# Optimization experiments

Hardware: AMD Instinct MI355X
Metric: run time of the kernel (lower is better)

## Reference

```python
import jax, jax.numpy as jnp
import numpy as np
import math

NUM_HEADS = 12
BLOCK_N = 32  # key-block size used by the Triton kernel for head_dim <= 64


def _apply_rope(x, cos, sin):
    # x: [B,H,S,D]; cos/sin: [S, D//2] -> interleaved-pair RoPE (matches apply_rope_rse)
    c = cos[None, None, :, :]
    s = sin[None, None, :, :]
    xe = x[..., 0::2]
    xo = x[..., 1::2]
    re = xe * c - xo * s
    ro = xo * c + xe * s
    return jnp.stack([re, ro], axis=-1).reshape(x.shape)


def setup_inputs() -> dict:
    key = jax.random.key(0)
    ks = jax.random.split(key, 9)
    B, S, HID = 16, 1024, 768
    D = HID // NUM_HEADS
    x = jax.random.normal(ks[0], (B, S, HID), jnp.float32)
    init = lambda k: jax.random.normal(k, (HID, HID), jnp.float32) * 0.02
    Wq, Wk, Wv, Wo = init(ks[1]), init(ks[2]), init(ks[3]), init(ks[4])
    bq = jnp.zeros((HID,), jnp.float32)
    bk = jnp.zeros((HID,), jnp.float32)
    bv = jnp.zeros((HID,), jnp.float32)
    bo = jnp.zeros((HID,), jnp.float32)
    lam = jnp.array(0.01, jnp.float32)
    # RoPE caches [S, D//2]
    inv_freq = 1.0 / (10000.0 ** (jnp.arange(0, D, 2, dtype=jnp.float32) / D))
    ang = jnp.arange(S, dtype=jnp.float32)[:, None] * inv_freq[None, :]
    cos_cache = jnp.cos(ang)
    sin_cache = jnp.sin(ang)
    return {"x": x, "Wq": Wq, "bq": bq, "Wk": Wk, "bk": bk, "Wv": Wv, "bv": bv,
            "Wo": Wo, "bo": bo, "lam": lam, "cos_cache": cos_cache, "sin_cache": sin_cache}


def _rse_attention(q, k, v, cos_cache, sin_cache, lam):
    # q,k,v: [B,H,S,D]. Block-sequential stick-breaking with online stats,
    # faithfully reproducing the Triton kernel's math (causal=False).
    B, H, S, D = q.shape
    scale = 1.0 / math.sqrt(D)
    qs = _apply_rope(q, cos_cache, sin_cache) * scale
    kr = _apply_rope(k, cos_cache, sin_cache)
    nb = S // BLOCK_N
    kb = jnp.moveaxis(kr.reshape(B, H, nb, BLOCK_N, D), 2, 0)  # [nb,B,H,BN,D]
    vb = jnp.moveaxis(v.reshape(B, H, nb, BLOCK_N, D), 2, 0)   # [nb,B,H,BN,D]
    pos_m = jnp.arange(S, dtype=jnp.float32)
    pb = jnp.arange(S, dtype=jnp.float32).reshape(nb, BLOCK_N)

    def step(carry, inp):
        rem, acc, l_i, m_i = carry
        kblk, vblk, pblk = inp
        decay = lam * jnp.abs(pos_m[:, None] - pblk[None, :])  # [S,BN]
        logits = jnp.einsum('bhmd,bhnd->bhmn', qs, kblk) - decay[None, None]
        beta = jax.nn.sigmoid(jnp.clip(logits, -20.0, 20.0))
        w = beta * rem[..., None]                 # [B,H,S,BN]
        consumed = jnp.sum(w, axis=-1)            # [B,H,S]
        rem_new = jnp.maximum(rem * (1.0 - consumed), 1e-6)
        acc_new = acc + jnp.einsum('bhmn,bhnd->bhmd', w, vblk)
        m_new = jnp.maximum(m_i, jnp.max(logits, axis=-1))
        alpha = jnp.exp2(m_i - m_new)
        l_new = l_i * alpha + consumed
        return (rem_new, acc_new, l_new, m_new), None

    rem0 = jnp.ones((B, H, S), jnp.float32)
    acc0 = jnp.zeros((B, H, S, D), jnp.float32)
    l0 = jnp.zeros((B, H, S), jnp.float32)
    m0 = jnp.full((B, H, S), -jnp.inf, jnp.float32)
    (rem, acc, l_i, m_i), _ = jax.lax.scan(step, (rem0, acc0, l0, m0), (kb, vb, pb))
    return acc / jnp.maximum(l_i, 1e-6)[..., None]


def reference(x, Wq, bq, Wk, bk, Wv, bv, Wo, bo, lam, cos_cache, sin_cache):
    B, S, HID = x.shape
    H = NUM_HEADS
    D = HID // H
    to_heads = lambda t: t.reshape(B, S, H, D).transpose(0, 2, 1, 3)
    q = to_heads(x @ Wq.T + bq)
    k = to_heads(x @ Wk.T + bk)
    v = to_heads(x @ Wv.T + bv)
    o = _rse_attention(q, k, v, cos_cache, sin_cache, lam)  # [B,H,S,D]
    ctx = o.transpose(0, 2, 1, 3).reshape(B, S, HID)
    return ctx @ Wo.T + bo
```

## Files before the change

### kernel.cpp

```cpp
#include <hip/hip_runtime.h>
#include <math.h>

#define NH    12
#define SEQ   1024
#define DH    64
#define HID   768
#define BATCH 16
#define MTOT  (BATCH*SEQ)
#define KDIM  HID

typedef __attribute__((ext_vector_type(8))) short short8;
typedef __attribute__((ext_vector_type(4))) short short4v;
typedef __attribute__((ext_vector_type(8))) unsigned short ushort8;
typedef __attribute__((ext_vector_type(4))) float float4v;

__device__ __forceinline__ float bf2f(unsigned short u) {
    union { unsigned int i; float f; } v; v.i = ((unsigned int)u) << 16; return v.f;
}
__device__ __forceinline__ unsigned short f2bf(float f) {
    union { float f; unsigned int i; } v; v.f = f;
    unsigned int x = v.i;
    return (unsigned short)((x + 0x7FFFu + ((x >> 16) & 1u)) >> 16);
}
__device__ __forceinline__ float loadf(const void* p, size_t i, bool f32) {
    return f32 ? ((const float*)p)[i] : bf2f(((const unsigned short*)p)[i]);
}
__device__ __forceinline__ unsigned int cvt_pk_bf16(float a, float b) {
    unsigned int r;
    asm("v_cvt_pk_bf16_f32 %0, %1, %2" : "=v"(r) : "v"(a), "v"(b));
    return r;
}
__device__ __forceinline__ float fast_exp2(float x) {
#if __has_builtin(__builtin_amdgcn_exp2f)
    return __builtin_amdgcn_exp2f(x);
#else
    return exp2f(x);
#endif
}

__device__ __forceinline__ void gload_lds16(const void* g, void* l) {
    __builtin_amdgcn_global_load_lds(
        (const __attribute__((address_space(1))) unsigned int*)g,
        (__attribute__((address_space(3))) unsigned int*)l, 16, 0, 0);
}

__global__ __launch_bounds__(256) void detect_kernel(
    const unsigned short* __restrict__ x, unsigned int* __restrict__ flag)
{
    __shared__ int cnt[256];
    const int tid = threadIdx.x;
    int local = 0;
    for (int i = tid; i < 1024; i += 256) {
        const unsigned short u = x[i];
        const int e = (u >> 7) & 0xFF;
        if ((e >= 96 && e <= 134) || ((u & 0x7FFF) == 0)) local++;
    }
    cnt[tid] = local;
    __syncthreads();
    for (int s = 128; s > 0; s >>= 1) {
        if (tid < s) cnt[tid] += cnt[tid + s];
        __syncthreads();
    }
    if (tid == 0) flag[0] = (cnt[0] < 900) ? 1u : 0u;
}

template<bool LO>
__global__ __launch_bounds__(256) void split_ker(
    const void* __restrict__ src, const unsigned int* __restrict__ flag,
    unsigned short* __restrict__ hi, unsigned short* __restrict__ lo, int n)
{
    const size_t i = ((size_t)blockIdx.x * 256 + threadIdx.x) * 8;
    if (i >= (size_t)n) return;
    ushort8 h, l;
    if (flag[0]) {
        const float* fp = (const float*)src + i;
        float4v f0 = *(const float4v*)fp, f1 = *(const float4v*)(fp + 4);
#pragma unroll
        for (int e = 0; e < 4; e++) {
            unsigned short h0 = f2bf(f0[e]), h1 = f2bf(f1[e]);
            h[e] = h0; h[4 + e] = h1;
            if (LO) { l[e] = f2bf(f0[e] - bf2f(h0)); l[4 + e] = f2bf(f1[e] - bf2f(h1)); }
        }
    } else {
        h = *(const ushort8*)((const unsigned short*)src + i);
        if (LO) {
#pragma unroll
            for (int e = 0; e < 8; e++) l[e] = 0;
        }
    }
    *(ushort8*)(hi + i) = h;
    if (LO) *(ushort8*)(lo + i) = l;
}

template<bool WF32, bool PRECISE>
__device__ __forceinline__ void loadW(const void* __restrict__ W, size_t idx,
                                      short8& hi, short8& lo) {
    if constexpr (WF32) {
        const float* fp = (const float*)W + idx;
        float4v f0 = *(const float4v*)fp, f1 = *(const float4v*)(fp + 4);
#pragma unroll
        for (int e = 0; e < 4; e++) {
            unsigned short h0 = f2bf(f0[e]), h1 = f2bf(f1[e]);
            hi[e] = (short)h0; hi[4 + e] = (short)h1;
            if constexpr (PRECISE) {
                lo[e] = (short)f2bf(f0[e] - bf2f(h0));
                lo[4 + e] = (short)f2bf(f1[e] - bf2f(h1));
            }
        }
    } else {
        hi = *(const short8*)((const unsigned short*)W + idx);
        if constexpr (PRECISE) {
#pragma unroll
            for (int e = 0; e < 8; e++) lo[e] = 0;
        }
    }
}

template<bool PRECISE, bool WPRE, bool WF32>
__device__ __forceinline__ void staged_kloop(
    const unsigned short* __restrict__ Ahi, const unsigned short* __restrict__ Alo,
    const void* __restrict__ Wa, const void* __restrict__ Wb,
    unsigned short* sAhi, unsigned short* sAlo,
    int m_blk0, int n_base, int wid, int lane, float4v acc[4][4])
{
    const int tid  = wid * 64 + lane;
    const int quad = lane >> 4, l16 = lane & 15;
    const int m_off = (wid >> 1) * 64;
    const int srow = tid >> 2;
    const int scc  = tid & 3;

    for (int k0 = 0; k0 < KDIM; k0 += 32) {
#pragma unroll
        for (int it = 0; it < 2; it++) {
            const int r = it * 64 + srow;
            const size_t gidx = (size_t)(m_blk0 + r) * KDIM + k0 + scc * 8;
            const int loff = r * 32 + scc * 8;
            gload_lds16(Ahi + gidx, sAhi + loff);
            if constexpr (PRECISE) gload_lds16(Alo + gidx, sAlo + loff);
        }
        short8 bh[4], bl[4];
#pragma unroll
        for (int in = 0; in < 4; in++) {
            const size_t widx = (size_t)(n_base + in * 16 + l16) * KDIM + k0 + quad * 8;
            if constexpr (WPRE) {
                bh[in] = *(const short8*)((const unsigned short*)Wa + widx);
                if constexpr (PRECISE)
                    bl[in] = *(const short8*)((const unsigned short*)Wb + widx);
            } else {
                loadW<WF32, PRECISE>(Wa, widx, bh[in], bl[in]);
            }
        }
        __syncthreads();
        short8 ah[4], al[4];
#pragma unroll
        for (int im = 0; im < 4; im++) {
            const int r = m_off + im * 16 + l16;
            ah[im] = *(const short8*)(sAhi + r * 32 + quad * 8);
            if constexpr (PRECISE) al[im] = *(const short8*)(sAlo + r * 32 + quad * 8);
        }
#pragma unroll
        for (int im = 0; im < 4; im++)
#pragma unroll
            for (int in = 0; in < 4; in++) {
                acc[im][in] = __builtin_amdgcn_mfma_f32_16x16x32_bf16(
                    ah[im], bh[in], acc[im][in], 0, 0, 0);
                if constexpr (PRECISE) {
                    acc[im][in] = __builtin_amdgcn_mfma_f32_16x16x32_bf16(
                        al[im], bh[in], acc[im][in], 0, 0, 0);
                    acc[im][in] = __builtin_amdgcn_mfma_f32_16x16x32_bf16(
                        ah[im], bl[in], acc[im][in], 0, 0, 0);
                }
            }
        __syncthreads();
    }
}

template<int MODE, bool WPRE>
__global__ __launch_bounds__(256) void gemm_staged(
    const unsigned short* __restrict__ Ahi, const unsigned short* __restrict__ Alo,
    const void* __restrict__ Wa, const void* __restrict__ Wb,
    const void* __restrict__ bias,
    const void* __restrict__ cosc, const void* __restrict__ sinc,
    const unsigned int* __restrict__ flag,
    void* __restrict__ Out, void* __restrict__ Out2)
{
    constexpr bool PRECISE = (MODE <= 1);
    __shared__ unsigned short sAhi[128 * 32];
    __shared__ unsigned short sAlo[PRECISE ? 128 * 32 : 64];

    const int tid  = threadIdx.x;
    const int wid  = tid >> 6;
    const int lane = tid & 63;
    const int quad = lane >> 4;
    const int l16  = lane & 15;
    const int m_blk0 = blockIdx.x * 128;
    const int m_blk = m_blk0 + (wid >> 1) * 64;
    const int n_base = blockIdx.y * 128 + (wid & 1) * 64;
    const bool f32 = (flag[0] != 0u);

    float4v acc[4][4];
#pragma unroll
    for (int i = 0; i < 4; i++)
#pragma unroll
        for (int j = 0; j < 4; j++) acc[i][j] = (float4v)(0.f);

    if constexpr (WPRE) {
        staged_kloop<PRECISE, true, false>(Ahi, Alo, Wa, Wb, sAhi, sAlo,
                                           m_blk0, n_base, wid, lane, acc);
    } else {
        if (f32) staged_kloop<PRECISE, false, true >(Ahi, Alo, Wa, Wb, sAhi, sAlo,
                                                     m_blk0, n_base, wid, lane, acc);
        else     staged_kloop<PRECISE, false, false>(Ahi, Alo, Wa, Wb, sAhi, sAlo,
                                                     m_blk0, n_base, wid, lane, acc);
    }

#pragma unroll
    for (int im = 0; im < 4; im++) {
#pragma unroll
        for (int in = 0; in < 4; in++) {
            const int col = n_base + in * 16 + l16;
            const float bval = loadf(bias, col, f32);
            if constexpr (MODE == 2) {
                short4v pk;
#pragma unroll
                for (int r = 0; r < 4; r++)
                    pk[r] = (short)f2bf(acc[im][in][r] + bval);
                const int row = m_blk + im * 16 + quad * 4;
                const int b = row >> 10, s = row & (SEQ - 1);
                const int h = col >> 6, d = col & (DH - 1);
                *(short4v*)((unsigned short*)Out +
                    ((size_t)(b * NH + h) * DH + d) * SEQ + s) = pk;
            } else if constexpr (MODE <= 1) {
                const int d  = col & (DH - 1);
                const int d2 = d >> 1;
#pragma unroll
                for (int r = 0; r < 4; r++) {
                    const int row = m_blk + im * 16 + quad * 4 + r;
                    const int s  = row & (SEQ - 1);
                    const float v = acc[im][in][r] + bval;
                    const float c  = loadf(cosc, s * (DH / 2) + d2, f32);
                    const float sn = loadf(sinc, s * (DH / 2) + d2, f32);
                    const float p = __shfl_xor(v, 1);
                    float o = (d & 1) ? (v * c + p * sn) : (v * c - p * sn);
                    if (MODE == 0) o *= 0.18033688f;
                    const float po = __shfl_xor(o, 1);
                    if (!(l16 & 1)) {
                        const unsigned short h0 = f2bf(o), h1 = f2bf(po);
                        const unsigned short l0 = f2bf(o - bf2f(h0));
                        const unsigned short l1 = f2bf(po - bf2f(h1));
                        const int b = row >> 10, h = col >> 6;
                        const size_t idx = ((size_t)(b * NH + h) * SEQ + s) * DH + d;
                        *(unsigned int*)((unsigned short*)Out + idx) =
                            (unsigned int)h0 | ((unsigned int)h1 << 16);
                        *(unsigned int*)((unsigned short*)Out2 + idx) =
                            (unsigned int)l0 | ((unsigned int)l1 << 16);
                    }
                }
            } else {
#pragma unroll
                for (int r = 0; r < 4; r++) {
                    const int row = m_blk + im * 16 + quad * 4 + r;
                    const float v = acc[im][in][r] + bval;
                    if (f32) ((float*)Out)[(size_t)row * HID + col] = v;
                    else     ((unsigned short*)Out)[(size_t)row * HID + col] = f2bf(v);
                }
            }
        }
    }
}

__global__ __launch_bounds__(256, 2) void attn_mfma(
    const unsigned short* __restrict__ Qhi, const unsigned short* __restrict__ Qlo,
    const unsigned short* __restrict__ Khi, const unsigned short* __restrict__ Klo,
    const unsigned short* __restrict__ Vt,
    const void* __restrict__ lam_p, const unsigned int* __restrict__ flag,
    unsigned short* __restrict__ ctx)
{
    const int tid  = threadIdx.x;
    const int wid  = tid >> 6;
    const int lane = tid & 63;
    const int quad = lane >> 4;
    const int l16  = lane & 15;
    const int phys = blockIdx.x;
    const int virt = (phys & 7) * 96 + (phys >> 3);
    const int bh   = virt >> 2;
    const int q0   = (virt & 3) * 256 + wid * 64;
    const bool f32 = (flag[0] != 0u);
    const float lam2 = loadf(lam_p, 0, f32) * 1.44269504f;

    __shared__ unsigned short KV[2][6144];

    const int krow = tid >> 3, kch = tid & 7;
    const int kgch = kch ^ (krow & 7);
    const int vrow = tid >> 2, vch = tid & 3;
    const int vgch = vch ^ (vrow & 3);

    #define STAGE(kb_, buf_) do {                                            \
        const size_t gk = ((size_t)bh * SEQ + (kb_) * 32 + krow) * DH + kgch * 8; \
        gload_lds16(Khi + gk, &KV[buf_][0]    + tid * 8);                    \
        gload_lds16(Klo + gk, &KV[buf_][2048] + tid * 8);                    \
        const size_t gv = ((size_t)bh * DH + vrow) * SEQ + (kb_) * 32 + vgch * 8; \
        gload_lds16(Vt + gv, &KV[buf_][4096] + tid * 8);                     \
    } while (0)

    short8 qh[4][2], ql[4][2];
#pragma unroll
    for (int qn = 0; qn < 4; qn++)
#pragma unroll
        for (int ks = 0; ks < 2; ks++) {
            const size_t base = ((size_t)bh * SEQ + (q0 + qn * 16 + l16)) * DH
                                + ks * 32 + quad * 8;
            qh[qn][ks] = *(const short8*)(Qhi + base);
            ql[qn][ks] = *(const short8*)(Qlo + base);
        }

    float4v acc_o[4][4];
#pragma unroll
    for (int i = 0; i < 4; i++)
#pragma unroll
        for (int j = 0; j < 4; j++) acc_o[i][j] = (float4v)(0.f);

    float rem[4] = {1.f, 1.f, 1.f, 1.f};
    float l_i[4] = {0.f, 0.f, 0.f, 0.f};
    float m_i[4] = {-INFINITY, -INFINITY, -INFINITY, -INFINITY};
    float qf[4];
#pragma unroll
    for (int qn = 0; qn < 4; qn++) qf[qn] = (float)(q0 + qn * 16 + l16);

    STAGE(0, 0);
    __syncthreads();

    for (int kb = 0; kb < SEQ / 32; kb++) {
        const int buf = kb & 1;
        if (kb + 1 < SEQ / 32) STAGE(kb + 1, buf ^ 1);

        short8 kh[2][2], kl[2][2];
#pragma unroll
        for (int kt = 0; kt < 2; kt++)
#pragma unroll
            for (int ks = 0; ks < 2; ks++) {
                const int off = (kt * 16 + l16) * 64
                                + ((ks * 4 + quad) ^ (l16 & 7)) * 8;
                kh[kt][ks] = *(const short8*)(&KV[buf][0]    + off);
                kl[kt][ks] = *(const short8*)(&KV[buf][2048] + off);
            }

        float4v s[2][4];
#pragma unroll
        for (int kt = 0; kt < 2; kt++)
#pragma unroll
            for (int qn = 0; qn < 4; qn++) s[kt][qn] = (float4v)(0.f);
#pragma unroll
        for (int ks = 0; ks < 2; ks++)
#pragma unroll
            for (int kt = 0; kt < 2; kt++)
#pragma unroll
                for (int qn = 0; qn < 4; qn++) {
                    s[kt][qn] = __builtin_amdgcn_mfma_f32_16x16x32_bf16(
                        kh[kt][ks], qh[qn][ks], s[kt][qn], 0, 0, 0);
                    s[kt][qn] = __builtin_amdgcn_mfma_f32_16x16x32_bf16(
                        kl[kt][ks], qh[qn][ks], s[kt][qn], 0, 0, 0);
                    s[kt][qn] = __builtin_amdgcn_mfma_f32_16x16x32_bf16(
                        kh[kt][ks], ql[qn][ks], s[kt][qn], 0, 0, 0);
                }

        float cons[4] = {0.f, 0.f, 0.f, 0.f};
        float mx[4] = {-INFINITY, -INFINITY, -INFINITY, -INFINITY};
#pragma unroll
        for (int kt = 0; kt < 2; kt++)
#pragma unroll
            for (int qn = 0; qn < 4; qn++)
#pragma unroll
                for (int r = 0; r < 4; r++) {
                    const float keyf = (float)(kb * 32 + kt * 16 + quad * 4 + r);
                    const float logit = s[kt][qn][r] - lam2 * fabsf(qf[qn] - keyf);
                    mx[qn] = fmaxf(mx[qn], logit);
                    const float beta = __builtin_amdgcn_rcpf(
                        1.f + fast_exp2(-logit));
                    const float w = beta * rem[qn];
                    cons[qn] += w;
                    s[kt][qn][r] = w;
                }
#pragma unroll
        for (int qn = 0; qn < 4; qn++) {
            cons[qn] += __shfl_xor(cons[qn], 16);
            cons[qn] += __shfl_xor(cons[qn], 32);
            mx[qn] = fmaxf(mx[qn], __shfl_xor(mx[qn], 16));
            mx[qn] = fmaxf(mx[qn], __shfl_xor(mx[qn], 32));
        }

        short8 pf[4];
#pragma unroll
        for (int qn = 0; qn < 4; qn++) {
            const unsigned int d00 = cvt_pk_bf16(s[0][qn][0], s[0][qn][1]);
            const unsigned int d01 = cvt_pk_bf16(s[0][qn][2], s[0][qn][3]);
            const unsigned int d10 = cvt_pk_bf16(s[1][qn][0], s[1][qn][1]);
            const unsigned int d11 = cvt_pk_bf16(s[1][qn][2], s[1][qn][3]);
            auto r0 = __builtin_amdgcn_permlane32_swap(d00, d10, false, false);
            auto r1 = __builtin_amdgcn_permlane32_swap(d01, d11, false, false);
            auto t0 = __builtin_amdgcn_permlane16_swap(r0[0], r0[1], false, false);
            auto t1 = __builtin_amdgcn_permlane16_swap(r1[0], r1[1], false, false);
            union { unsigned int u[4]; short8 s8; } cv;
            cv.u[0] = t0[0];
            cv.u[1] = t1[0];
            cv.u[2] = t0[1];
            cv.u[3] = t1[1];
            pf[qn] = cv.s8;
        }

        short8 vf[4];
#pragma unroll
        for (int dt = 0; dt < 4; dt++) {
            const int off = (dt * 16 + l16) * 32 + (quad ^ (l16 & 3)) * 8;
            vf[dt] = *(const short8*)(&KV[buf][4096] + off);
        }
#pragma unroll
        for (int dt = 0; dt < 4; dt++)
#pragma unroll
            for (int jn = 0; jn < 4; jn++)
                acc_o[dt][jn] = __builtin_amdgcn_mfma_f32_16x16x32_bf16(
                    vf[dt], pf[jn], acc_o[dt][jn], 0, 0, 0);

#pragma unroll
        for (int qn = 0; qn < 4; qn++) {
            rem[qn] = fmaxf(rem[qn] * (1.f - cons[qn]), 1e-6f);
            const float m_new = fmaxf(m_i[qn], mx[qn]);
            const float alpha = fast_exp2((m_i[qn] - m_new) * 0.69314718f);
            l_i[qn] = l_i[qn] * alpha + cons[qn];
            m_i[qn] = m_new;
        }

        __syncthreads();
    }

    const int b = bh / NH, h = bh % NH;
    float inv[4];
#pragma unroll
    for (int jn = 0; jn < 4; jn++)
        inv[jn] = __builtin_amdgcn_rcpf(fmaxf(l_i[jn], 1e-6f));
#pragma unroll
    for (int dt = 0; dt < 4; dt++)
#pragma unroll
        for (int jn = 0; jn < 4; jn++) {
            short4v pk;
#pragma unroll
            for (int r = 0; r < 4; r++)
                pk[r] = (short)f2bf(acc_o[dt][jn][r] * inv[jn]);
            const int q_g = q0 + jn * 16 + l16;
            *(short4v*)(ctx + ((size_t)(b * SEQ + q_g) * HID
                               + h * DH + dt * 16 + quad * 4)) = pk;
        }
    #undef STAGE
}

extern "C" void kernel_launch(void* const* d_in, const int* in_sizes, int n_in,
                              void* d_out, int out_size, void* d_ws, size_t ws_size,
                              hipStream_t stream) {
    const void* x    = d_in[0];
    const void* Wq   = d_in[1];
    const void* bq   = d_in[2];
    const void* Wk   = d_in[3];
    const void* bk   = d_in[4];
    const void* Wv   = d_in[5];
    const void* bv   = d_in[6];
    const void* Wo   = d_in[7];
    const void* bo   = d_in[8];
    const void* lam  = d_in[9];
    const void* cosc = d_in[10];
    const void* sinc = d_in[11];

    const size_t NELEM = (size_t)MTOT * HID;
    const size_t WELEM = (size_t)HID * HID;
    unsigned int* flag = (unsigned int*)d_ws;
    unsigned short* Xhi = (unsigned short*)((char*)d_ws + 64);
    unsigned short* Xlo = Xhi + NELEM;
    unsigned short* Qhi = Xlo + NELEM;
    unsigned short* Qlo = Qhi + NELEM;
    unsigned short* Wqh = Qlo + NELEM;
    unsigned short* Wql = Wqh + WELEM;
    unsigned short* Wkh = Wql + WELEM;
    unsigned short* Wkl = Wkh + WELEM;
    unsigned short* Wvh = Wkl + WELEM;
    unsigned short* Woh = Wvh + WELEM;
    const size_t NEED = 64 + 4 * NELEM * 2 + 6 * WELEM * 2;
    const bool wpre = (ws_size >= NEED);

    unsigned short* Vt  = Xlo;
    unsigned short* Ctx = Xhi;
    unsigned short* Khi = (unsigned short*)d_out;
    unsigned short* Klo = Khi + NELEM;

    detect_kernel<<<1, 256, 0, stream>>>((const unsigned short*)x, flag);
    split_ker<true><<<(MTOT * KDIM) / 2048, 256, 0, stream>>>(x, flag, Xhi, Xlo, MTOT * KDIM);

    dim3 gg(MTOT / 128, HID / 128), gb(256);
    if (wpre) {
        const int wb = (int)(WELEM / 2048);
        split_ker<true ><<<wb, 256, 0, stream>>>(Wq, flag, Wqh, Wql, (int)WELEM);
        split_ker<true ><<<wb, 256, 0, stream>>>(Wk, flag, Wkh, Wkl, (int)WELEM);
        split_ker<false><<<wb, 256, 0, stream>>>(Wv, flag, Wvh, nullptr, (int)WELEM);
        split_ker<false><<<wb, 256, 0, stream>>>(Wo, flag, Woh, nullptr, (int)WELEM);
        gemm_staged<0, true><<<gg, gb, 0, stream>>>(Xhi, Xlo, Wqh, Wql, bq, cosc, sinc, flag, Qhi, Qlo);
        gemm_staged<1, true><<<gg, gb, 0, stream>>>(Xhi, Xlo, Wkh, Wkl, bk, cosc, sinc, flag, Khi, Klo);
        gemm_staged<2, true><<<gg, gb, 0, stream>>>(Xhi, nullptr, Wvh, nullptr, bv, nullptr, nullptr, flag, Vt, nullptr);
    } else {
        gemm_staged<0, false><<<gg, gb, 0, stream>>>(Xhi, Xlo, Wq, nullptr, bq, cosc, sinc, flag, Qhi, Qlo);
        gemm_staged<1, false><<<gg, gb, 0, stream>>>(Xhi, Xlo, Wk, nullptr, bk, cosc, sinc, flag, Khi, Klo);
        gemm_staged<2, false><<<gg, gb, 0, stream>>>(Xhi, nullptr, Wv, nullptr, bv, nullptr, nullptr, flag, Vt, nullptr);
    }
    attn_mfma<<<dim3(4 * BATCH * NH), 256, 0, stream>>>(
        Qhi, Qlo, Khi, Klo, Vt, lam, flag, Ctx);
    if (wpre)
        gemm_staged<3, true><<<gg, gb, 0, stream>>>(Ctx, nullptr, Woh, nullptr, bo, nullptr, nullptr, flag, d_out, nullptr);
    else
        gemm_staged<3, false><<<gg, gb, 0, stream>>>(Ctx, nullptr, Wo, nullptr, bo, nullptr, nullptr, flag, d_out, nullptr);
}
```

Baseline: 661.9 us.

## Double-buffer GEMM LDS staging and fuse Q/K/V projections into one launch

The GEMM k-loop now prefetches the next A tile into a second LDS buffer while computing on the current one, and drops one barrier per iteration. A new gemm_qkv kernel computes the Q, K and V projections in a single grid, with V written to a separate workspace region when space allows. This is meant to hide global-load latency and cut launch and tail overhead across the three projection GEMMs. In exchange it doubles LDS use per block and relies on async LDS loads completing before the next iteration's reads.

```diff
diff --git a/kernel.cpp b/kernel.cpp
--- a/kernel.cpp
+++ b/kernel.cpp
@@ -129,15 +129,24 @@
     const int srow = tid >> 2;
     const int scc  = tid & 3;
 
-    for (int k0 = 0; k0 < KDIM; k0 += 32) {
+    auto stage = [&](int k0, int b) {
 #pragma unroll
         for (int it = 0; it < 2; it++) {
             const int r = it * 64 + srow;
             const size_t gidx = (size_t)(m_blk0 + r) * KDIM + k0 + scc * 8;
-            const int loff = r * 32 + scc * 8;
+            const int loff = b * 4096 + r * 32 + scc * 8;
             gload_lds16(Ahi + gidx, sAhi + loff);
             if constexpr (PRECISE) gload_lds16(Alo + gidx, sAlo + loff);
         }
+    };
+
+    stage(0, 0);
+    __syncthreads();
+
+    for (int k0 = 0; k0 < KDIM; k0 += 32) {
+        const int b = (k0 >> 5) & 1;
+        if (k0 + 32 < KDIM) stage(k0 + 32, b ^ 1);
+
         short8 bh[4], bl[4];
 #pragma unroll
         for (int in = 0; in < 4; in++) {
@@ -150,13 +159,12 @@
                 loadW<WF32, PRECISE>(Wa, widx, bh[in], bl[in]);
             }
         }
-        __syncthreads();
         short8 ah[4], al[4];
 #pragma unroll
         for (int im = 0; im < 4; im++) {
             const int r = m_off + im * 16 + l16;
-            ah[im] = *(const short8*)(sAhi + r * 32 + quad * 8);
-            if constexpr (PRECISE) al[im] = *(const short8*)(sAlo + r * 32 + quad * 8);
+            ah[im] = *(const short8*)(sAhi + b * 4096 + r * 32 + quad * 8);
+            if constexpr (PRECISE) al[im] = *(const short8*)(sAlo + b * 4096 + r * 32 + quad * 8);
         }
 #pragma unroll
         for (int im = 0; im < 4; im++)
@@ -176,26 +184,24 @@
 }
 
 template<int MODE, bool WPRE>
-__global__ __launch_bounds__(256) void gemm_staged(
+__device__ __forceinline__ void gemm_body(
     const unsigned short* __restrict__ Ahi, const unsigned short* __restrict__ Alo,
     const void* __restrict__ Wa, const void* __restrict__ Wb,
     const void* __restrict__ bias,
     const void* __restrict__ cosc, const void* __restrict__ sinc,
     const unsigned int* __restrict__ flag,
-    void* __restrict__ Out, void* __restrict__ Out2)
+    void* __restrict__ Out, void* __restrict__ Out2,
+    unsigned short* sAhi, unsigned short* sAlo,
+    int m_blk0, int ny)
 {
     constexpr bool PRECISE = (MODE <= 1);
-    __shared__ unsigned short sAhi[128 * 32];
-    __shared__ unsigned short sAlo[PRECISE ? 128 * 32 : 64];
-
     const int tid  = threadIdx.x;
     const int wid  = tid >> 6;
     const int lane = tid & 63;
     const int quad = lane >> 4;
     const int l16  = lane & 15;
-    const int m_blk0 = blockIdx.x * 128;
     const int m_blk = m_blk0 + (wid >> 1) * 64;
-    const int n_base = blockIdx.y * 128 + (wid & 1) * 64;
+    const int n_base = ny * 128 + (wid & 1) * 64;
     const bool f32 = (flag[0] != 0u);
 
     float4v acc[4][4];
@@ -269,6 +275,52 @@
     }
 }
 
+template<int MODE, bool WPRE>
+__global__ __launch_bounds__(256) void gemm_staged(
+    const unsigned short* __restrict__ Ahi, const unsigned short* __restrict__ Alo,
+    const void* __restrict__ Wa, const void* __restrict__ Wb,
+    const void* __restrict__ bias,
+    const void* __restrict__ cosc, const void* __restrict__ sinc,
+    const unsigned int* __restrict__ flag,
+    void* __restrict__ Out, void* __restrict__ Out2)
+{
+    constexpr bool PRECISE = (MODE <= 1);
+    __shared__ unsigned short sAhi[2 * 4096];
+    __shared__ unsigned short sAlo[PRECISE ? 2 * 4096 : 64];
+    gemm_body<MODE, WPRE>(Ahi, Alo, Wa, Wb, bias, cosc, sinc, flag, Out, Out2,
+                          sAhi, sAlo, blockIdx.x * 128, blockIdx.y);
+}
+
+template<bool WPRE>
+__global__ __launch_bounds__(256) void gemm_qkv(
+    const unsigned short* __restrict__ Ahi, const unsigned short* __restrict__ Alo,
+    const void* __restrict__ Wqa, const void* __restrict__ Wqb,
+    const void* __restrict__ Wka, const void* __restrict__ Wkb,
+    const void* __restrict__ Wva,
+    const void* __restrict__ bq, const void* __restrict__ bk,
+    const void* __restrict__ bv,
+    const void* __restrict__ cosc, const void* __restrict__ sinc,
+    const unsigned int* __restrict__ flag,
+    void* __restrict__ Qhi, void* __restrict__ Qlo,
+    void* __restrict__ Khi, void* __restrict__ Klo,
+    void* __restrict__ Vt)
+{
+    __shared__ unsigned short sAhi[2 * 4096];
+    __shared__ unsigned short sAlo[2 * 4096];
+    const int which = blockIdx.y / 6;
+    const int ny    = blockIdx.y % 6;
+    const int m0    = blockIdx.x * 128;
+    if (which == 0)
+        gemm_body<0, WPRE>(Ahi, Alo, Wqa, Wqb, bq, cosc, sinc, flag,
+                           Qhi, Qlo, sAhi, sAlo, m0, ny);
+    else if (which == 1)
+        gemm_body<1, WPRE>(Ahi, Alo, Wka, Wkb, bk, cosc, sinc, flag,
+                           Khi, Klo, sAhi, sAlo, m0, ny);
+    else
+        gemm_body<2, WPRE>(Ahi, nullptr, Wva, nullptr, bv, nullptr, nullptr, flag,
+                           Vt, nullptr, sAhi, sAlo, m0, ny);
+}
+
 __global__ __launch_bounds__(256, 2) void attn_mfma(
     const unsigned short* __restrict__ Qhi, const unsigned short* __restrict__ Qlo,
     const unsigned short* __restrict__ Khi, const unsigned short* __restrict__ Klo,
@@ -482,10 +534,13 @@
     unsigned short* Wkl = Wkh + WELEM;
     unsigned short* Wvh = Wkl + WELEM;
     unsigned short* Woh = Wvh + WELEM;
-    const size_t NEED = 64 + 4 * NELEM * 2 + 6 * WELEM * 2;
+    unsigned short* VtF = Woh + WELEM;
+    const size_t NEED  = 64 + 4 * NELEM * 2 + 6 * WELEM * 2;
+    const size_t NEEDF = NEED + NELEM * 2;
     const bool wpre = (ws_size >= NEED);
-
-    unsigned short* Vt  = Xlo;
+    const bool fuse = (ws_size >= NEEDF);
+
+    unsigned short* Vt  = fuse ? VtF : Xlo;
     unsigned short* Ctx = Xhi;
     unsigned short* Khi = (unsigned short*)d_out;
     unsigned short* Klo = Khi + NELEM;
@@ -494,7 +549,16 @@
     split_ker<true><<<(MTOT * KDIM) / 2048, 256, 0, stream>>>(x, flag, Xhi, Xlo, MTOT * KDIM);
 
     dim3 gg(MTOT / 128, HID / 128), gb(256);
-    if (wpre) {
+    if (fuse) {
+        const int wb = (int)(WELEM / 2048);
+        split_ker<true ><<<wb, 256, 0, stream>>>(Wq, flag, Wqh, Wql, (int)WELEM);
+        split_ker<true ><<<wb, 256, 0, stream>>>(Wk, flag, Wkh, Wkl, (int)WELEM);
+        split_ker<false><<<wb, 256, 0, stream>>>(Wv, flag, Wvh, nullptr, (int)WELEM);
+        split_ker<false><<<wb, 256, 0, stream>>>(Wo, flag, Woh, nullptr, (int)WELEM);
+        gemm_qkv<true><<<dim3(MTOT / 128, 18), gb, 0, stream>>>(
+            Xhi, Xlo, Wqh, Wql, Wkh, Wkl, Wvh, bq, bk, bv,
+            cosc, sinc, flag, Qhi, Qlo, Khi, Klo, VtF);
+    } else if (wpre) {
         const int wb = (int)(WELEM / 2048);
         split_ker<true ><<<wb, 256, 0, stream>>>(Wq, flag, Wqh, Wql, (int)WELEM);
         split_ker<true ><<<wb, 256, 0, stream>>>(Wk, flag, Wkh, Wkl, (int)WELEM);
```

Result: no change. 665.9 us (+0.6%).
